# Optimization experiments

Measured on AMD Instinct MI355X. Metric: run time of the kernel, lower is better.

## Reference

```python
import jax, jax.numpy as jnp
import numpy as np

RATIO = 4
K_TOP = 2

def setup_inputs() -> dict:
    key = jax.random.key(0)
    k1, k2 = jax.random.split(key)
    B, C, H, W = 4, 128, 128, 128
    N_low = (H // RATIO) * (W // RATIO)
    v_high_feat = jax.random.normal(k1, (B, C, H, W), dtype=jnp.float32)
    coarse_attn_map = jax.random.normal(k2, (B, N_low, N_low), dtype=jnp.float32)
    return {"v_high_feat": v_high_feat, "coarse_attn_map": coarse_attn_map}

def reference(v_high_feat, coarse_attn_map):
    ratio, k = RATIO, K_TOP
    B, C, H, W = v_high_feat.shape
    H_low, W_low = H // ratio, W // ratio
    N_high, N_low = H * W, H_low * W_low
    r2 = ratio * ratio

    # [B, N_high, C]
    v_seq = v_high_feat.reshape(B, C, N_high).transpose(0, 2, 1)

    # top-k over coarse attention rows: [B, N_low, k]
    topk_values, topk_idx = jax.lax.top_k(coarse_attn_map, k)

    # low-res 2d coords of top-k keys, scaled to high-res top-left corners
    tl_row = (topk_idx // W_low) * ratio  # [B, N_low, k]
    tl_col = (topk_idx % W_low) * ratio

    # r x r patch offsets: [r2, 2]
    dr, dc = jnp.meshgrid(jnp.arange(ratio), jnp.arange(ratio), indexing='ij')
    drow, dcol = dr.reshape(-1), dc.reshape(-1)

    # flattened high-res indices per (low query, sample, patch cell): [B, N_low, k*r2]
    sparse_row = tl_row[..., None] + drow  # [B, N_low, k, r2]
    sparse_col = tl_col[..., None] + dcol
    sparse_1d = (sparse_row * W + sparse_col).reshape(B, N_low, k * r2)

    # each high-res query maps to its containing low-res cell: [N_high]
    qr, qc = jnp.meshgrid(jnp.arange(H), jnp.arange(W), indexing='ij')
    low_idx = ((qr // ratio) * W_low + (qc // ratio)).reshape(N_high)

    # broadcast low-res sample indices/weights to every high-res query
    final_idx = sparse_1d[:, low_idx, :]  # [B, N_high, k*r2]

    # gather sampled values: [B, N_high, k*r2, C]
    batch_idx = jnp.arange(B)[:, None, None]
    v_sparse = v_seq[batch_idx, final_idx]

    # softmax weights over k samples, gathered to high-res queries
    w_low = jax.nn.softmax(topk_values, axis=-1)  # [B, N_low, k]
    w_high = w_low[:, low_idx, :]                 # [B, N_high, k]

    v_r = v_sparse.reshape(B, N_high, k, r2, C)
    w = (w_high / r2)[..., None, None]            # [B, N_high, k, 1, 1]
    warped_seq = (v_r * w).sum(axis=(2, 3))       # [B, N_high, C]

    return warped_seq.transpose(0, 2, 1).reshape(B, C, H, W)
```

## Files before the change

### kernel.cpp

```cpp
#include <hip/hip_runtime.h>
#include <float.h>

#define B_ 4
#define C_ 128
#define H_ 128
#define W_ 128
#define WL_ 32
#define NL_ 1024

__global__ __launch_bounds__(256) void k_top2(const float* __restrict__ attn,
                                              int2* __restrict__ tmap,
                                              float2* __restrict__ wmap) {
    int lane = threadIdx.x & 63;
    int wv   = threadIdx.x >> 6;
    int row  = blockIdx.x * 4 + wv;
    const float4* p = (const float4*)(attn + (size_t)row * NL_);

    float v0 = -FLT_MAX, v1 = -FLT_MAX;
    int   i0 = 0x7fffffff, i1 = 0x7fffffff;

    #pragma unroll
    for (int s = 0; s < 4; ++s) {
        float4 u = p[lane + 64 * s];
        int j = 4 * (lane + 64 * s);
        float vals[4] = {u.x, u.y, u.z, u.w};
        #pragma unroll
        for (int t = 0; t < 4; ++t) {
            float a = vals[t];
            int   ji = j + t;
            if (a > v0)      { v1 = v0; i1 = i0; v0 = a; i0 = ji; }
            else if (a > v1) { v1 = a; i1 = ji; }
        }
    }

    #pragma unroll
    for (int off = 32; off >= 1; off >>= 1) {
        float ov0 = __shfl_xor(v0, off, 64);
        int   oi0 = __shfl_xor(i0, off, 64);
        float ov1 = __shfl_xor(v1, off, 64);
        int   oi1 = __shfl_xor(i1, off, 64);
        bool a_first = (v0 > ov0) || (v0 == ov0 && i0 < oi0);
        float n0, n1; int m0, m1;
        if (a_first) {
            n0 = v0; m0 = i0;
            bool s2 = (v1 > ov0) || (v1 == ov0 && i1 < oi0);
            n1 = s2 ? v1 : ov0; m1 = s2 ? i1 : oi0;
        } else {
            n0 = ov0; m0 = oi0;
            bool s2 = (v0 > ov1) || (v0 == ov1 && i0 < oi1);
            n1 = s2 ? v0 : ov1; m1 = s2 ? i0 : oi1;
        }
        v0 = n0; i0 = m0; v1 = n1; i1 = m1;
    }

    if (lane == 0) {
        float e  = expf(v1 - v0);
        float w0 = 1.f / (1.f + e);
        tmap[row] = make_int2(i0, i1);
        wmap[row] = make_float2(w0, 1.f - w0);
    }
}

__global__ __launch_bounds__(1024) void k_plane(const float* __restrict__ v,
                                                const int2* __restrict__ tmap,
                                                const float2* __restrict__ wmap,
                                                float* __restrict__ out) {
    __shared__ float S_l[NL_];
    int plane = blockIdx.x;
    int b   = plane >> 7;
    int tid = threadIdx.x;

    {
        int cr = tid >> 5, cc = tid & 31;
        const float* rp = v + (size_t)plane * (H_ * W_) + (cr * 4) * W_ + cc * 4;
        float s = 0.f;
        #pragma unroll
        for (int r = 0; r < 4; ++r) {
            float4 u = *(const float4*)(rp + r * W_);
            s += u.x + u.y + u.z + u.w;
        }
        S_l[tid] = s;
    }
    __syncthreads();

    {
        int2   t = tmap[b * NL_ + tid];
        float2 w = wmap[b * NL_ + tid];
        float val = (w.x * S_l[t.x] + w.y * S_l[t.y]) * 0.0625f;

        int ht = tid >> 5, wb = tid & 31;
        float4 o4 = make_float4(val, val, val, val);
        float* op = out + ((size_t)plane * H_ + ht * 4) * W_ + wb * 4;
        #pragma unroll
        for (int r = 0; r < 4; ++r)
            *(float4*)(op + r * W_) = o4;
    }
}

extern "C" void kernel_launch(void* const* d_in, const int* in_sizes, int n_in,
                              void* d_out, int out_size, void* d_ws, size_t ws_size,
                              hipStream_t stream) {
    const float* v    = (const float*)d_in[0];
    const float* attn = (const float*)d_in[1];
    float* out = (float*)d_out;

    char* base = (char*)d_ws;
    int2*   tmap = (int2*)base;
    float2* wmap = (float2*)(base + 4096 * sizeof(int2));

    k_top2<<<1024, 256, 0, stream>>>(attn, tmap, wmap);
    k_plane<<<B_ * C_, 1024, 0, stream>>>(v, tmap, wmap, out);
}
```

Measured before the change: 95.37 us.

## Fuse top-2 selection and plane pooling into one cooperative kernel with grid sync

Merges the top-2 kernel and the per-plane pooling kernel into a single cooperative launch of 512 blocks. Each block pools its plane into shared memory, computes top-2 for 8 attention rows, then waits on a grid-wide barrier before reading the maps and writing output. The aim is to remove one kernel launch and overlap the attention reads with the feature reads. In exchange it pays for a grid-wide barrier and requires all 512 blocks of 1024 threads to be co-resident. If the cooperative launch fails it falls back to the two-kernel path.

```diff
diff --git a/kernel.cpp b/kernel.cpp
--- a/kernel.cpp
+++ b/kernel.cpp
@@ -1,4 +1,5 @@
 #include <hip/hip_runtime.h>
+#include <hip/hip_cooperative_groups.h>
 #include <float.h>
 
 #define B_ 4
@@ -8,12 +9,12 @@
 #define WL_ 32
 #define NL_ 1024
 
-__global__ __launch_bounds__(256) void k_top2(const float* __restrict__ attn,
-                                              int2* __restrict__ tmap,
-                                              float2* __restrict__ wmap) {
-    int lane = threadIdx.x & 63;
-    int wv   = threadIdx.x >> 6;
-    int row  = blockIdx.x * 4 + wv;
+namespace cg = cooperative_groups;
+
+__device__ __forceinline__ void top2_row(const float* __restrict__ attn,
+                                         int row, int lane,
+                                         int2* __restrict__ tmap,
+                                         float2* __restrict__ wmap) {
     const float4* p = (const float4*)(attn + (size_t)row * NL_);
 
     float v0 = -FLT_MAX, v1 = -FLT_MAX;
@@ -61,11 +62,13 @@
     }
 }
 
-__global__ __launch_bounds__(1024) void k_plane(const float* __restrict__ v,
-                                                const int2* __restrict__ tmap,
-                                                const float2* __restrict__ wmap,
-                                                float* __restrict__ out) {
+__global__ __launch_bounds__(1024, 8) void k_all(const float* __restrict__ v,
+                                                 const float* __restrict__ attn,
+                                                 int2* __restrict__ tmap,
+                                                 float2* __restrict__ wmap,
+                                                 float* __restrict__ out) {
     __shared__ float S_l[NL_];
+    cg::grid_group grid = cg::this_grid();
     int plane = blockIdx.x;
     int b   = plane >> 7;
     int tid = threadIdx.x;
@@ -81,13 +84,61 @@
         }
         S_l[tid] = s;
     }
-    __syncthreads();
+
+    {
+        int lane = tid & 63;
+        int wv   = tid >> 6;
+        if (wv < 8)
+            top2_row(attn, blockIdx.x * 8 + wv, lane, tmap, wmap);
+    }
+
+    grid.sync();
 
     {
         int2   t = tmap[b * NL_ + tid];
         float2 w = wmap[b * NL_ + tid];
         float val = (w.x * S_l[t.x] + w.y * S_l[t.y]) * 0.0625f;
 
+        int ht = tid >> 5, wb = tid & 31;
+        float4 o4 = make_float4(val, val, val, val);
+        float* op = out + ((size_t)plane * H_ + ht * 4) * W_ + wb * 4;
+        #pragma unroll
+        for (int r = 0; r < 4; ++r)
+            *(float4*)(op + r * W_) = o4;
+    }
+}
+
+__global__ __launch_bounds__(256) void k_top2(const float* __restrict__ attn,
+                                              int2* __restrict__ tmap,
+                                              float2* __restrict__ wmap) {
+    top2_row(attn, blockIdx.x * 4 + (threadIdx.x >> 6), threadIdx.x & 63,
+             tmap, wmap);
+}
+
+__global__ __launch_bounds__(1024) void k_plane(const float* __restrict__ v,
+                                                const int2* __restrict__ tmap,
+                                                const float2* __restrict__ wmap,
+                                                float* __restrict__ out) {
+    __shared__ float S_l[NL_];
+    int plane = blockIdx.x;
+    int b   = plane >> 7;
+    int tid = threadIdx.x;
+    {
+        int cr = tid >> 5, cc = tid & 31;
+        const float* rp = v + (size_t)plane * (H_ * W_) + (cr * 4) * W_ + cc * 4;
+        float s = 0.f;
+        #pragma unroll
+        for (int r = 0; r < 4; ++r) {
+            float4 u = *(const float4*)(rp + r * W_);
+            s += u.x + u.y + u.z + u.w;
+        }
+        S_l[tid] = s;
+    }
+    __syncthreads();
+    {
+        int2   t = tmap[b * NL_ + tid];
+        float2 w = wmap[b * NL_ + tid];
+        float val = (w.x * S_l[t.x] + w.y * S_l[t.y]) * 0.0625f;
         int ht = tid >> 5, wb = tid & 31;
         float4 o4 = make_float4(val, val, val, val);
         float* op = out + ((size_t)plane * H_ + ht * 4) * W_ + wb * 4;
@@ -108,6 +159,13 @@
     int2*   tmap = (int2*)base;
     float2* wmap = (float2*)(base + 4096 * sizeof(int2));
 
-    k_top2<<<1024, 256, 0, stream>>>(attn, tmap, wmap);
-    k_plane<<<B_ * C_, 1024, 0, stream>>>(v, tmap, wmap, out);
+    void* args[] = {(void*)&v, (void*)&attn, (void*)&tmap, (void*)&wmap,
+                    (void*)&out};
+    hipError_t err = hipLaunchCooperativeKernel((void*)k_all,
+                                                dim3(B_ * C_), dim3(1024),
+                                                args, 0, stream);
+    if (err != hipSuccess) {
+        k_top2<<<1024, 256, 0, stream>>>(attn, tmap, wmap);
+        k_plane<<<B_ * C_, 1024, 0, stream>>>(v, tmap, wmap, out);
+    }
 }
```

Measured after the change: 141.0 us. +47.8%, slower.
